# Kernel tuning notes

Hardware: AMD Instinct MI355X
Metric: run time of the kernel (lower is better)

Reference implementation:

```python
import jax, jax.numpy as jnp
import numpy as np

N = 50000   # nodes
E = 600000  # edges
D = 128     # input_dim
H = 128     # hidden_dim
C = 1       # num_classes
EPS = 1e-5


def _glorot(key, fan_in, fan_out):
    s = (2.0 / (fan_in + fan_out)) ** 0.5
    return jax.random.normal(key, (fan_in, fan_out), jnp.float32) * s


def setup_inputs() -> dict:
    key = jax.random.key(0)
    ks = jax.random.split(key, 16)
    inp = {
        "x": jax.random.normal(ks[0], (N, D), jnp.float32),
        "edge_index": jax.random.randint(ks[1], (2, E), 0, N, dtype=jnp.int64),
        # GCN layer 0: D -> H, layers 1,2: H -> H
        "W0": _glorot(ks[2], D, H), "b0": jnp.zeros((H,), jnp.float32),
        "g0": jnp.ones((H,), jnp.float32), "be0": jnp.zeros((H,), jnp.float32),
        "W1": _glorot(ks[3], H, H), "b1": jnp.zeros((H,), jnp.float32),
        "g1": jnp.ones((H,), jnp.float32), "be1": jnp.zeros((H,), jnp.float32),
        "W2": _glorot(ks[4], H, H), "b2": jnp.zeros((H,), jnp.float32),
        "g2": jnp.ones((H,), jnp.float32), "be2": jnp.zeros((H,), jnp.float32),
        # MLP head: Linear(H,H) -> ReLU -> Linear(H,C)
        "hW1": _glorot(ks[5], H, H), "hb1": jnp.zeros((H,), jnp.float32),
        "hW2": _glorot(ks[6], H, C), "hb2": jnp.zeros((C,), jnp.float32),
    }
    return inp


def _layer_norm(h, g, b):
    mu = jnp.mean(h, axis=-1, keepdims=True)
    var = jnp.mean(jnp.square(h - mu), axis=-1, keepdims=True)
    return (h - mu) * jax.lax.rsqrt(var + EPS) * g + b


def reference(x, edge_index, W0, b0, g0, be0, W1, b1, g1, be1, W2, b2, g2, be2,
              hW1, hb1, hW2, hb2):
    # --- GCN normalization (add self-loops, symmetric deg^-1/2 norm) ---
    loop = jnp.arange(N, dtype=edge_index.dtype)
    src = jnp.concatenate([edge_index[0], loop])  # [E+N]
    dst = jnp.concatenate([edge_index[1], loop])  # [E+N]
    deg = jax.ops.segment_sum(jnp.ones_like(dst, jnp.float32), dst, num_segments=N)
    dinv = jax.lax.rsqrt(deg)  # deg >= 1 due to self-loops
    norm = (dinv[src] * dinv[dst])[:, None]  # [E+N, 1]

    def gcn_layer(h, W, b, g, be):
        hW = h @ W                                   # [N, H] dense GEMM
        msg = hW[src] * norm                         # gather + scale  [E+N, H]
        agg = jax.ops.segment_sum(msg, dst, num_segments=N) + b
        return jax.nn.relu(_layer_norm(agg, g, be))  # dropout = identity (eval)

    h = gcn_layer(x, W0, b0, g0, be0)
    h = gcn_layer(h, W1, b1, g1, be1)
    h = gcn_layer(h, W2, b2, g2, be2)

    # MLP head
    h = jax.nn.relu(h @ hW1 + hb1)
    logits = h @ hW2 + hb2  # [N, C]
    return logits
```

## Files before the change

kernel.cpp:

```cpp
#include <hip/hip_runtime.h>
#include <hip/hip_fp16.h>

#define N_NODES 50000
#define N_EDGES 600000
#define HDIM 128
#define EPS 1e-5f
#define ELLW 64
#define LPADH 136

typedef __attribute__((ext_vector_type(4))) float f32x4;
typedef __attribute__((ext_vector_type(4))) _Float16 h16x4;
typedef __attribute__((ext_vector_type(8))) _Float16 h16x8;

#define EDGE_BLKS ((N_EDGES + 255) / 256)
#define CVT_BLKS 6250
#define PACK_BLKS 32

__global__ void detect_kernel(const int* __restrict__ ei, int* __restrict__ flag) {
    __shared__ int nonzero;
    if (threadIdx.x == 0) nonzero = 0;
    __syncthreads();
    int acc = 0;
    for (int i = threadIdx.x; i < 1024; i += blockDim.x)
        acc |= ei[2 * i + 1];
    if (acc) atomicOr(&nonzero, 1);
    __syncthreads();
    if (threadIdx.x == 0) *flag = (nonzero == 0) ? 1 : 0;
}

__device__ __forceinline__ int load_idx(const int* __restrict__ ei, int pos, int f) {
    return f ? ei[2 * pos] : ei[pos];
}

__device__ __forceinline__ void hsplit(float a, _Float16& hi, _Float16& lo) {
    _Float16 h = (_Float16)a;
    hi = h;
    lo = (_Float16)(a - (float)h);
}

__global__ void prep_kernel(const float* __restrict__ x, _Float16* __restrict__ xh,
                            const int* __restrict__ ei, const int* __restrict__ flag,
                            int* __restrict__ deg, unsigned short* __restrict__ ell,
                            const float* __restrict__ W0, const float* __restrict__ W1,
                            const float* __restrict__ W2, const float* __restrict__ W3,
                            _Float16* __restrict__ pkh, _Float16* __restrict__ pkl) {
    int b = blockIdx.x;
    if (b < EDGE_BLKS) {
        int e = b * 256 + threadIdx.x;
        if (e < N_EDGES) {
            int f = *flag;
            int s = load_idx(ei, e, f);
            int d = load_idx(ei, N_EDGES + e, f);
            int pos = atomicAdd(&deg[d], 1);
            if (pos < ELLW) ell[(size_t)d * ELLW + pos] = (unsigned short)s;
        }
    } else if (b < EDGE_BLKS + CVT_BLKS) {
        int idx = (b - EDGE_BLKS) * 256 + threadIdx.x;
        if (idx < N_NODES * 32) {
            float4 v = ((const float4*)x)[idx];
            h16x4 o;
            o[0] = (_Float16)v.x; o[1] = (_Float16)v.y;
            o[2] = (_Float16)v.z; o[3] = (_Float16)v.w;
            ((h16x4*)xh)[idx] = o;
        }
    } else {
        int pb = b - EDGE_BLKS - CVT_BLKS;
        int wsel = pb >> 3;
        const float* W = (wsel == 0) ? W0 : (wsel == 1) ? W1 : (wsel == 2) ? W2 : W3;
        int idx = (pb & 7) * 256 + threadIdx.x;
        int lane = idx & 63;
        int cf = (idx >> 6) & 7;
        int ks = idx >> 9;
        int col = cf * 16 + (lane & 15);
        int k0 = ks * 32 + (lane >> 4) * 8;
        _Float16 h[8], l[8];
#pragma unroll
        for (int i = 0; i < 8; ++i) hsplit(W[(size_t)(k0 + i) * HDIM + col], h[i], l[i]);
        size_t base = (size_t)wsel * 16384 + (size_t)idx * 8;
#pragma unroll
        for (int i = 0; i < 8; ++i) { pkh[base + i] = h[i]; pkl[base + i] = l[i]; }
    }
}

__global__ __launch_bounds__(256) void layer_fused(const _Float16* __restrict__ h,
                                                   const int* __restrict__ deg,
                                                   const unsigned short* __restrict__ ell,
                                                   const _Float16* __restrict__ Bh,
                                                   const _Float16* __restrict__ Bl,
                                                   const float* __restrict__ bias,
                                                   const float* __restrict__ gamma,
                                                   const float* __restrict__ beta,
                                                   _Float16* __restrict__ out, int nrows) {
    __shared__ _Float16 As[64][LPADH];
    int t = threadIdx.x;
    int blockRow = blockIdx.x * 64;

    {
        int g = t >> 4, sub = t & 15;
        const h16x8* h8 = (const h16x8*)h;
        for (int j = 0; j < 4; ++j) {
            int rl = j * 16 + g;
            int node = blockRow + rl;
            h16x8 r;
            if (node < nrows) {
                int dn = deg[node];
                float dd = rsqrtf((float)dn + 1.0f);
                h16x8 v = h8[(size_t)node * 16 + sub];
                float acc[8];
#pragma unroll
                for (int i = 0; i < 8; ++i) acc[i] = dd * (float)v[i];
                int cnt = min(dn, ELLW);
                const unsigned short* row = ell + (size_t)node * ELLW;
                for (int e = 0; e < cnt; e += 4) {
                    uint2 pk = *(const uint2*)(row + e);
                    int s0 = (int)(pk.x & 0xFFFFu);
                    int s1 = (int)(pk.x >> 16);
                    int s2 = (int)(pk.y & 0xFFFFu);
                    int s3 = (int)(pk.y >> 16);
                    bool k1 = e + 1 < cnt, k2 = e + 2 < cnt, k3 = e + 3 < cnt;
                    s1 = k1 ? s1 : s0;
                    s2 = k2 ? s2 : s0;
                    s3 = k3 ? s3 : s0;
                    int d0 = deg[s0];
                    int d1 = deg[s1];
                    int d2 = deg[s2];
                    int d3 = deg[s3];
                    h16x8 u0 = h8[(size_t)s0 * 16 + sub];
                    h16x8 u1 = h8[(size_t)s1 * 16 + sub];
                    h16x8 u2 = h8[(size_t)s2 * 16 + sub];
                    h16x8 u3 = h8[(size_t)s3 * 16 + sub];
                    float w0 = rsqrtf((float)d0 + 1.0f);
                    float w1 = k1 ? rsqrtf((float)d1 + 1.0f) : 0.f;
                    float w2 = k2 ? rsqrtf((float)d2 + 1.0f) : 0.f;
                    float w3 = k3 ? rsqrtf((float)d3 + 1.0f) : 0.f;
#pragma unroll
                    for (int i = 0; i < 8; ++i) {
                        acc[i] += w0 * (float)u0[i];
                        acc[i] += w1 * (float)u1[i];
                        acc[i] += w2 * (float)u2[i];
                        acc[i] += w3 * (float)u3[i];
                    }
                }
#pragma unroll
                for (int i = 0; i < 8; ++i) r[i] = (_Float16)(acc[i] * dd);
            } else {
#pragma unroll
                for (int i = 0; i < 8; ++i) r[i] = (_Float16)0.f;
            }
            *(h16x8*)&As[rl][sub * 8] = r;
        }
    }
    __syncthreads();

    int wave = t >> 6, lane = t & 63;
    int lrow = lane & 15, lk = lane >> 4;
    int rowb = blockRow + wave * 16;

    f32x4 acc[8];
#pragma unroll
    for (int cf = 0; cf < 8; ++cf) acc[cf] = (f32x4){0.f, 0.f, 0.f, 0.f};

#pragma unroll
    for (int ks = 0; ks < 4; ++ks) {
        h16x8 a = *(const h16x8*)&As[wave * 16 + lrow][ks * 32 + lk * 8];
        const _Float16* bhp = Bh + (size_t)(ks * 8) * 512 + (size_t)lane * 8;
        const _Float16* blp = Bl + (size_t)(ks * 8) * 512 + (size_t)lane * 8;
#pragma unroll
        for (int cf = 0; cf < 8; ++cf) {
            h16x8 bh = *(const h16x8*)(bhp + (size_t)cf * 512);
            h16x8 bl = *(const h16x8*)(blp + (size_t)cf * 512);
            acc[cf] = __builtin_amdgcn_mfma_f32_16x16x32_f16(a, bh, acc[cf], 0, 0, 0);
            acc[cf] = __builtin_amdgcn_mfma_f32_16x16x32_f16(a, bl, acc[cf], 0, 0, 0);
        }
    }

    float bias_v[8], gam[8], bet[8];
#pragma unroll
    for (int cf = 0; cf < 8; ++cf) {
        bias_v[cf] = bias[cf * 16 + lrow];
        gam[cf] = gamma[cf * 16 + lrow];
        bet[cf] = beta[cf * 16 + lrow];
    }
#pragma unroll
    for (int r = 0; r < 4; ++r) {
        float vv[8];
        float s1 = 0.f;
#pragma unroll
        for (int cf = 0; cf < 8; ++cf) {
            vv[cf] = acc[cf][r] + bias_v[cf];
            s1 += vv[cf];
        }
#pragma unroll
        for (int m = 1; m <= 8; m <<= 1) s1 += __shfl_xor(s1, m);
        float mean = s1 * (1.0f / 128.0f);
        float s2 = 0.f;
        float cc[8];
#pragma unroll
        for (int cf = 0; cf < 8; ++cf) {
            cc[cf] = vv[cf] - mean;
            s2 += cc[cf] * cc[cf];
        }
#pragma unroll
        for (int m = 1; m <= 8; m <<= 1) s2 += __shfl_xor(s2, m);
        float var = s2 * (1.0f / 128.0f);
        float rs = rsqrtf(var + EPS);
        int row = rowb + lk * 4 + r;
        if (row < nrows) {
#pragma unroll
            for (int cf = 0; cf < 8; ++cf) {
                float y = cc[cf] * rs * gam[cf] + bet[cf];
                out[(size_t)row * HDIM + cf * 16 + lrow] = (_Float16)(y > 0.f ? y : 0.f);
            }
        }
    }
}

__global__ __launch_bounds__(256) void head_mfma(const _Float16* __restrict__ A,
                                                 const _Float16* __restrict__ Bh,
                                                 const _Float16* __restrict__ Bl,
                                                 const float* __restrict__ bias,
                                                 const float* __restrict__ w2,
                                                 const float* __restrict__ b2p,
                                                 float* __restrict__ out, int nrows) {
    int t = threadIdx.x;
    int wave = t >> 6, lane = t & 63;
    int lrow = lane & 15, lk = lane >> 4;
    int rowb = blockIdx.x * 64 + wave * 16;

    f32x4 acc[8];
#pragma unroll
    for (int cf = 0; cf < 8; ++cf) acc[cf] = (f32x4){0.f, 0.f, 0.f, 0.f};

    const _Float16* arow = A + (size_t)(rowb + lrow) * HDIM;
#pragma unroll
    for (int ks = 0; ks < 4; ++ks) {
        h16x8 a = *(const h16x8*)(arow + ks * 32 + lk * 8);
        const _Float16* bhp = Bh + (size_t)(ks * 8) * 512 + (size_t)lane * 8;
        const _Float16* blp = Bl + (size_t)(ks * 8) * 512 + (size_t)lane * 8;
#pragma unroll
        for (int cf = 0; cf < 8; ++cf) {
            h16x8 bh = *(const h16x8*)(bhp + (size_t)cf * 512);
            h16x8 bl = *(const h16x8*)(blp + (size_t)cf * 512);
            acc[cf] = __builtin_amdgcn_mfma_f32_16x16x32_f16(a, bh, acc[cf], 0, 0, 0);
            acc[cf] = __builtin_amdgcn_mfma_f32_16x16x32_f16(a, bl, acc[cf], 0, 0, 0);
        }
    }

    float bias_v[8], w2v[8];
#pragma unroll
    for (int cf = 0; cf < 8; ++cf) {
        bias_v[cf] = bias[cf * 16 + lrow];
        w2v[cf] = w2[cf * 16 + lrow];
    }
    float b2 = b2p[0];
#pragma unroll
    for (int r = 0; r < 4; ++r) {
        float part = 0.f;
#pragma unroll
        for (int cf = 0; cf < 8; ++cf) {
            float y = acc[cf][r] + bias_v[cf];
            y = y > 0.f ? y : 0.f;
            part += y * w2v[cf];
        }
#pragma unroll
        for (int m = 1; m <= 8; m <<= 1) part += __shfl_xor(part, m);
        int row = rowb + lk * 4 + r;
        if (row < nrows && lrow == 0) out[row] = part + b2;
    }
}

extern "C" void kernel_launch(void* const* d_in, const int* in_sizes, int n_in,
                              void* d_out, int out_size, void* d_ws, size_t ws_size,
                              hipStream_t stream) {
    (void)in_sizes; (void)n_in; (void)out_size; (void)ws_size;
    const float* x   = (const float*)d_in[0];
    const int*   ei  = (const int*)d_in[1];
    const float* W0  = (const float*)d_in[2];
    const float* b0  = (const float*)d_in[3];
    const float* g0  = (const float*)d_in[4];
    const float* be0 = (const float*)d_in[5];
    const float* W1  = (const float*)d_in[6];
    const float* b1  = (const float*)d_in[7];
    const float* g1  = (const float*)d_in[8];
    const float* be1 = (const float*)d_in[9];
    const float* W2  = (const float*)d_in[10];
    const float* b2  = (const float*)d_in[11];
    const float* g2  = (const float*)d_in[12];
    const float* be2 = (const float*)d_in[13];
    const float* hW1 = (const float*)d_in[14];
    const float* hb1 = (const float*)d_in[15];
    const float* hW2 = (const float*)d_in[16];
    const float* hb2 = (const float*)d_in[17];
    float* out = (float*)d_out;

    char* w = (char*)d_ws;
    size_t off = 0;
    auto alloc = [&](size_t bytes) -> void* {
        void* p = w + off;
        off += (bytes + 255) & ~(size_t)255;
        return p;
    };
    int*            deg  = (int*)alloc((size_t)N_NODES * 4);
    unsigned short* ell  = (unsigned short*)alloc((size_t)N_NODES * ELLW * 2);
    int*            flag = (int*)alloc(256);
    _Float16*       xh   = (_Float16*)alloc((size_t)N_NODES * HDIM * 2);
    _Float16*       hA   = (_Float16*)alloc((size_t)N_NODES * HDIM * 2);
    _Float16*       hB   = (_Float16*)alloc((size_t)N_NODES * HDIM * 2);
    _Float16*       pkh  = (_Float16*)alloc((size_t)4 * 16384 * 2);
    _Float16*       pkl  = (_Float16*)alloc((size_t)4 * 16384 * 2);

    hipMemsetAsync(deg, 0, (size_t)N_NODES * 4, stream);

    detect_kernel<<<1, 256, 0, stream>>>(ei, flag);
    prep_kernel<<<EDGE_BLKS + CVT_BLKS + PACK_BLKS, 256, 0, stream>>>(
        x, xh, ei, flag, deg, ell, W0, W1, W2, hW1, pkh, pkl);

    int ngb = (N_NODES + 63) / 64;
    layer_fused<<<ngb, 256, 0, stream>>>(xh, deg, ell, pkh, pkl, b0, g0, be0, hA, N_NODES);
    layer_fused<<<ngb, 256, 0, stream>>>(hA, deg, ell, pkh + (size_t)16384, pkl + (size_t)16384,
                                         b1, g1, be1, hB, N_NODES);
    layer_fused<<<ngb, 256, 0, stream>>>(hB, deg, ell, pkh + (size_t)2 * 16384, pkl + (size_t)2 * 16384,
                                         b2, g2, be2, hA, N_NODES);
    head_mfma<<<ngb, 256, 0, stream>>>(hA, pkh + (size_t)3 * 16384, pkl + (size_t)3 * 16384,
                                       hb1, hW2, hb2, out, N_NODES);
}
```

Baseline: 172.2 us.

## Fold first-layer GEMM into prep kernel and aggregate with a gather-only kernel

The first GCN layer now computes x@W0 inside the prep kernel, concurrently with edge bucketing: x is converted to fp16 on the fly and W0 is split into hi/lo halves inline. This replaces the separate x-to-fp16 conversion and W0 packing. A new agg_ln kernel then performs only the normalized neighbor gather, bias, LayerNorm and ReLU on the precomputed product. The deg memset is folded into the detect kernel, which removes a launch. The GEMM blocks reread W0 from global memory per block, and layer 0 now aggregates after the transform, matching the reference order.

```diff
diff --git a/kernel.cpp b/kernel.cpp
--- a/kernel.cpp
+++ b/kernel.cpp
@@ -13,19 +13,24 @@
 typedef __attribute__((ext_vector_type(8))) _Float16 h16x8;
 
 #define EDGE_BLKS ((N_EDGES + 255) / 256)
-#define CVT_BLKS 6250
-#define PACK_BLKS 32
-
-__global__ void detect_kernel(const int* __restrict__ ei, int* __restrict__ flag) {
-    __shared__ int nonzero;
-    if (threadIdx.x == 0) nonzero = 0;
-    __syncthreads();
-    int acc = 0;
-    for (int i = threadIdx.x; i < 1024; i += blockDim.x)
-        acc |= ei[2 * i + 1];
-    if (acc) atomicOr(&nonzero, 1);
-    __syncthreads();
-    if (threadIdx.x == 0) *flag = (nonzero == 0) ? 1 : 0;
+#define GEMM0_BLKS ((N_NODES + 63) / 64)
+#define PACK_BLKS 24
+
+__global__ void detect_zero(const int* __restrict__ ei, int* __restrict__ flag,
+                            int* __restrict__ deg) {
+    int i = blockIdx.x * 256 + threadIdx.x;
+    if (i < N_NODES) deg[i] = 0;
+    if (blockIdx.x == 0) {
+        __shared__ int nonzero;
+        if (threadIdx.x == 0) nonzero = 0;
+        __syncthreads();
+        int acc = 0;
+        for (int k = threadIdx.x; k < 1024; k += 256)
+            acc |= ei[2 * k + 1];
+        if (acc) atomicOr(&nonzero, 1);
+        __syncthreads();
+        if (threadIdx.x == 0) *flag = (nonzero == 0) ? 1 : 0;
+    }
 }
 
 __device__ __forceinline__ int load_idx(const int* __restrict__ ei, int pos, int f) {
@@ -38,11 +43,12 @@
     lo = (_Float16)(a - (float)h);
 }
 
-__global__ void prep_kernel(const float* __restrict__ x, _Float16* __restrict__ xh,
+__global__ void prep_kernel(const float* __restrict__ x,
                             const int* __restrict__ ei, const int* __restrict__ flag,
                             int* __restrict__ deg, unsigned short* __restrict__ ell,
-                            const float* __restrict__ W0, const float* __restrict__ W1,
-                            const float* __restrict__ W2, const float* __restrict__ W3,
+                            const float* __restrict__ W0, _Float16* __restrict__ y0,
+                            const float* __restrict__ W1, const float* __restrict__ W2,
+                            const float* __restrict__ W3,
                             _Float16* __restrict__ pkh, _Float16* __restrict__ pkl) {
     int b = blockIdx.x;
     if (b < EDGE_BLKS) {
@@ -54,19 +60,60 @@
             int pos = atomicAdd(&deg[d], 1);
             if (pos < ELLW) ell[(size_t)d * ELLW + pos] = (unsigned short)s;
         }
-    } else if (b < EDGE_BLKS + CVT_BLKS) {
-        int idx = (b - EDGE_BLKS) * 256 + threadIdx.x;
-        if (idx < N_NODES * 32) {
-            float4 v = ((const float4*)x)[idx];
-            h16x4 o;
-            o[0] = (_Float16)v.x; o[1] = (_Float16)v.y;
-            o[2] = (_Float16)v.z; o[3] = (_Float16)v.w;
-            ((h16x4*)xh)[idx] = o;
+    } else if (b < EDGE_BLKS + GEMM0_BLKS) {
+        int gb = b - EDGE_BLKS;
+        int t = threadIdx.x;
+        int wave = t >> 6, lane = t & 63;
+        int lrow = lane & 15, lk = lane >> 4;
+        int rowb = gb * 64 + wave * 16;
+        int arowi = rowb + lrow;
+        f32x4 acc[8];
+#pragma unroll
+        for (int cf = 0; cf < 8; ++cf) acc[cf] = (f32x4){0.f, 0.f, 0.f, 0.f};
+        const float* arow = x + (size_t)arowi * HDIM;
+        bool aok = arowi < N_NODES;
+#pragma unroll
+        for (int ks = 0; ks < 4; ++ks) {
+            h16x8 a;
+            if (aok) {
+                float4 a0 = *(const float4*)(arow + ks * 32 + lk * 8);
+                float4 a1 = *(const float4*)(arow + ks * 32 + lk * 8 + 4);
+                a[0] = (_Float16)a0.x; a[1] = (_Float16)a0.y;
+                a[2] = (_Float16)a0.z; a[3] = (_Float16)a0.w;
+                a[4] = (_Float16)a1.x; a[5] = (_Float16)a1.y;
+                a[6] = (_Float16)a1.z; a[7] = (_Float16)a1.w;
+            } else {
+#pragma unroll
+                for (int i = 0; i < 8; ++i) a[i] = (_Float16)0.f;
+            }
+            int k0 = ks * 32 + lk * 8;
+#pragma unroll
+            for (int cf = 0; cf < 8; ++cf) {
+                int col = cf * 16 + lrow;
+                h16x8 bh, bl;
+#pragma unroll
+                for (int i = 0; i < 8; ++i) {
+                    _Float16 hh, ll;
+                    hsplit(W0[(size_t)(k0 + i) * HDIM + col], hh, ll);
+                    bh[i] = hh; bl[i] = ll;
+                }
+                acc[cf] = __builtin_amdgcn_mfma_f32_16x16x32_f16(a, bh, acc[cf], 0, 0, 0);
+                acc[cf] = __builtin_amdgcn_mfma_f32_16x16x32_f16(a, bl, acc[cf], 0, 0, 0);
+            }
+        }
+#pragma unroll
+        for (int r = 0; r < 4; ++r) {
+            int row = rowb + lk * 4 + r;
+            if (row < N_NODES) {
+#pragma unroll
+                for (int cf = 0; cf < 8; ++cf)
+                    y0[(size_t)row * HDIM + cf * 16 + lrow] = (_Float16)acc[cf][r];
+            }
         }
     } else {
-        int pb = b - EDGE_BLKS - CVT_BLKS;
+        int pb = b - EDGE_BLKS - GEMM0_BLKS;
         int wsel = pb >> 3;
-        const float* W = (wsel == 0) ? W0 : (wsel == 1) ? W1 : (wsel == 2) ? W2 : W3;
+        const float* W = (wsel == 0) ? W1 : (wsel == 1) ? W2 : W3;
         int idx = (pb & 7) * 256 + threadIdx.x;
         int lane = idx & 63;
         int cf = (idx >> 6) & 7;
@@ -80,6 +127,93 @@
 #pragma unroll
         for (int i = 0; i < 8; ++i) { pkh[base + i] = h[i]; pkl[base + i] = l[i]; }
     }
+}
+
+__global__ __launch_bounds__(256) void agg_ln(const _Float16* __restrict__ y0,
+                                              const int* __restrict__ deg,
+                                              const unsigned short* __restrict__ ell,
+                                              const float* __restrict__ bias,
+                                              const float* __restrict__ gamma,
+                                              const float* __restrict__ beta,
+                                              _Float16* __restrict__ out) {
+    int node = blockIdx.x * 16 + (threadIdx.x >> 4);
+    int sub = threadIdx.x & 15;
+    if (node >= N_NODES) return;
+    const h16x8* h8 = (const h16x8*)y0;
+    int dn = deg[node];
+    float dd = rsqrtf((float)dn + 1.0f);
+    h16x8 v = h8[(size_t)node * 16 + sub];
+    float acc[8];
+#pragma unroll
+    for (int i = 0; i < 8; ++i) acc[i] = dd * (float)v[i];
+    int cnt = min(dn, ELLW);
+    const unsigned short* row = ell + (size_t)node * ELLW;
+    for (int j = 0; j < cnt; j += 4) {
+        uint2 pk = *(const uint2*)(row + j);
+        int s0 = (int)(pk.x & 0xFFFFu);
+        int s1 = (int)(pk.x >> 16);
+        int s2 = (int)(pk.y & 0xFFFFu);
+        int s3 = (int)(pk.y >> 16);
+        bool k1 = j + 1 < cnt, k2 = j + 2 < cnt, k3 = j + 3 < cnt;
+        s1 = k1 ? s1 : s0;
+        s2 = k2 ? s2 : s0;
+        s3 = k3 ? s3 : s0;
+        int d0 = deg[s0];
+        int d1 = deg[s1];
+        int d2 = deg[s2];
+        int d3 = deg[s3];
+        h16x8 u0 = h8[(size_t)s0 * 16 + sub];
+        h16x8 u1 = h8[(size_t)s1 * 16 + sub];
+        h16x8 u2 = h8[(size_t)s2 * 16 + sub];
+        h16x8 u3 = h8[(size_t)s3 * 16 + sub];
+        float w0 = rsqrtf((float)d0 + 1.0f);
+        float w1 = k1 ? rsqrtf((float)d1 + 1.0f) : 0.f;
+        float w2 = k2 ? rsqrtf((float)d2 + 1.0f) : 0.f;
+        float w3 = k3 ? rsqrtf((float)d3 + 1.0f) : 0.f;
+#pragma unroll
+        for (int i = 0; i < 8; ++i) {
+            acc[i] += w0 * (float)u0[i];
+            acc[i] += w1 * (float)u1[i];
+            acc[i] += w2 * (float)u2[i];
+            acc[i] += w3 * (float)u3[i];
+        }
+    }
+    float4 bi0 = *(const float4*)&bias[sub * 8];
+    float4 bi1 = *(const float4*)&bias[sub * 8 + 4];
+    float bv[8] = {bi0.x, bi0.y, bi0.z, bi0.w, bi1.x, bi1.y, bi1.z, bi1.w};
+    float vv[8];
+    float s1v = 0.f;
+#pragma unroll
+    for (int i = 0; i < 8; ++i) {
+        vv[i] = acc[i] * dd + bv[i];
+        s1v += vv[i];
+    }
+#pragma unroll
+    for (int m = 1; m <= 8; m <<= 1) s1v += __shfl_xor(s1v, m);
+    float mean = s1v * (1.0f / 128.0f);
+    float s2v = 0.f;
+    float cc[8];
+#pragma unroll
+    for (int i = 0; i < 8; ++i) {
+        cc[i] = vv[i] - mean;
+        s2v += cc[i] * cc[i];
+    }
+#pragma unroll
+    for (int m = 1; m <= 8; m <<= 1) s2v += __shfl_xor(s2v, m);
+    float rs = rsqrtf(s2v * (1.0f / 128.0f) + EPS);
+    float4 g0 = *(const float4*)&gamma[sub * 8];
+    float4 g1 = *(const float4*)&gamma[sub * 8 + 4];
+    float4 e0 = *(const float4*)&beta[sub * 8];
+    float4 e1 = *(const float4*)&beta[sub * 8 + 4];
+    float gv[8] = {g0.x, g0.y, g0.z, g0.w, g1.x, g1.y, g1.z, g1.w};
+    float ev[8] = {e0.x, e0.y, e0.z, e0.w, e1.x, e1.y, e1.z, e1.w};
+    h16x8 r;
+#pragma unroll
+    for (int i = 0; i < 8; ++i) {
+        float y = cc[i] * rs * gv[i] + ev[i];
+        r[i] = (_Float16)(y > 0.f ? y : 0.f);
+    }
+    ((h16x8*)out)[(size_t)node * 16 + sub] = r;
 }
 
 __global__ __launch_bounds__(256) void layer_fused(const _Float16* __restrict__ h,
@@ -202,8 +336,7 @@
         }
 #pragma unroll
         for (int m = 1; m <= 8; m <<= 1) s2 += __shfl_xor(s2, m);
-        float var = s2 * (1.0f / 128.0f);
-        float rs = rsqrtf(var + EPS);
+        float rs = rsqrtf(s2 * (1.0f / 128.0f) + EPS);
         int row = rowb + lk * 4 + r;
         if (row < nrows) {
 #pragma unroll
@@ -303,24 +436,22 @@
     int*            deg  = (int*)alloc((size_t)N_NODES * 4);
     unsigned short* ell  = (unsigned short*)alloc((size_t)N_NODES * ELLW * 2);
     int*            flag = (int*)alloc(256);
-    _Float16*       xh   = (_Float16*)alloc((size_t)N_NODES * HDIM * 2);
+    _Float16*       y0   = (_Float16*)alloc((size_t)N_NODES * HDIM * 2);
     _Float16*       hA   = (_Float16*)alloc((size_t)N_NODES * HDIM * 2);
     _Float16*       hB   = (_Float16*)alloc((size_t)N_NODES * HDIM * 2);
-    _Float16*       pkh  = (_Float16*)alloc((size_t)4 * 16384 * 2);
-    _Float16*       pkl  = (_Float16*)alloc((size_t)4 * 16384 * 2);
-
-    hipMemsetAsync(deg, 0, (size_t)N_NODES * 4, stream);
-
-    detect_kernel<<<1, 256, 0, stream>>>(ei, flag);
-    prep_kernel<<<EDGE_BLKS + CVT_BLKS + PACK_BLKS, 256, 0, stream>>>(
-        x, xh, ei, flag, deg, ell, W0, W1, W2, hW1, pkh, pkl);
-
+    _Float16*       pkh  = (_Float16*)alloc((size_t)3 * 16384 * 2);
+    _Float16*       pkl  = (_Float16*)alloc((size_t)3 * 16384 * 2);
+
+    detect_zero<<<(N_NODES + 255) / 256, 256, 0, stream>>>(ei, flag, deg);
+    prep_kernel<<<EDGE_BLKS + GEMM0_BLKS + PACK_BLKS, 256, 0, stream>>>(
+        x, ei, flag, deg, ell, W0, y0, W1, W2, hW1, pkh, pkl);
+
+    int nab = (N_NODES + 15) / 16;
     int ngb = (N_NODES + 63) / 64;
-    layer_fused<<<ngb, 256, 0, stream>>>(xh, deg, ell, pkh, pkl, b0, g0, be0, hA, N_NODES);
-    layer_fused<<<ngb, 256, 0, stream>>>(hA, deg, ell, pkh + (size_t)16384, pkl + (size_t)16384,
-                                         b1, g1, be1, hB, N_NODES);
-    layer_fused<<<ngb, 256, 0, stream>>>(hB, deg, ell, pkh + (size_t)2 * 16384, pkl + (size_t)2 * 16384,
+    agg_ln<<<nab, 256, 0, stream>>>(y0, deg, ell, b0, g0, be0, hA);
+    layer_fused<<<ngb, 256, 0, stream>>>(hA, deg, ell, pkh, pkl, b1, g1, be1, hB, N_NODES);
+    layer_fused<<<ngb, 256, 0, stream>>>(hB, deg, ell, pkh + (size_t)16384, pkl + (size_t)16384,
                                          b2, g2, be2, hA, N_NODES);
-    head_mfma<<<ngb, 256, 0, stream>>>(hA, pkh + (size_t)3 * 16384, pkl + (size_t)3 * 16384,
+    head_mfma<<<ngb, 256, 0, stream>>>(hA, pkh + (size_t)2 * 16384, pkl + (size_t)2 * 16384,
                                        hb1, hW2, hb2, out, N_NODES);
 }
```

After: 175.1 us. About the same (+1.7%).
